# Performance work log

Measured on AMD Instinct MI355X. Metric: run time of the kernel, lower is better.

The kernel has to match this reference:

```python
import jax, jax.numpy as jnp
import numpy as np

B, S, HID = 1, 2048, 2048
H = 16
DN, DR, DV = 128, 64, 128          # qk_nope_head_dim, qk_rope_head_dim, v_head_dim
DQ = DN + DR                        # q_head_dim = 192
QLR, KVLR = 1536, 512               # q_lora_rank, kv_lora_rank
MAXP = 32 * 1024
SCALE = DQ ** -0.5
EPS = 1e-6


def rmsnorm(x, w):
    return x * jax.lax.rsqrt(jnp.mean(x * x, axis=-1, keepdims=True) + EPS) * w


def rotate_half(x):
    h = x.shape[-1] // 2
    return jnp.concatenate((-x[..., h:], x[..., :h]), axis=-1)


def interleave_to_half(x):
    # torch: view(b,h,s,d//2,2).transpose(4,3).reshape(b,h,s,d)
    b, h, s, d = x.shape
    return x.reshape(b, h, s, d // 2, 2).transpose(0, 1, 2, 4, 3).reshape(b, h, s, d)


def setup_inputs() -> dict:
    key = jax.random.key(0)
    ks = jax.random.split(key, 8)
    def w(k, shape):
        fan_in = shape[-1]
        return jax.random.normal(k, shape, jnp.float32) * (fan_in ** -0.5)
    inp = {
        "hidden_states": jax.random.normal(ks[0], (B, S, HID), jnp.float32),
        "q_a_w": w(ks[1], (QLR, HID)),
        "q_a_ln": jnp.ones((QLR,), jnp.float32),
        "q_b_w": w(ks[2], (H * DQ, QLR)),
        "kv_a_w": w(ks[3], (KVLR + DR, HID)),
        "kv_a_ln": jnp.ones((KVLR,), jnp.float32),
        "kv_b_w": w(ks[4], (H * (DN + DV), KVLR)),
        "o_w": w(ks[5], (HID, H * DV)),
    }
    # rotary tables, seq_len = 32k
    inv_freq = 1.0 / (10000.0 ** (np.arange(0, DR, 2, dtype=np.float32) / DR))
    t = np.arange(MAXP, dtype=np.float32)
    freqs = np.outer(t, inv_freq)
    emb = np.concatenate((freqs, freqs), axis=-1)
    inp["cos"] = jnp.asarray(np.cos(emb), jnp.float32)
    inp["sin"] = jnp.asarray(np.sin(emb), jnp.float32)
    # bool mask, True = masked (causal)
    inp["attention_mask"] = jnp.triu(jnp.ones((S, S), bool), 1)[None, None]
    inp["position_ids"] = jnp.arange(S, dtype=jnp.int64 if jax.config.jax_enable_x64 else jnp.int32)[None].repeat(B, 0)
    return inp


def reference(hidden_states, q_a_w, q_a_ln, q_b_w, kv_a_w, kv_a_ln, kv_b_w, o_w,
              cos, sin, attention_mask, position_ids):
    b, s, _ = hidden_states.shape
    # low-rank Q: q_b(LN(q_a(x)))
    q = rmsnorm(hidden_states @ q_a_w.T, q_a_ln) @ q_b_w.T         # [b,s,H*DQ]
    q = q.reshape(b, s, H, DQ).transpose(0, 2, 1, 3)               # [b,H,s,DQ]
    q_nope, q_pe = q[..., :DN], q[..., DN:]
    # compressed KV + decoupled rope key
    ckv = hidden_states @ kv_a_w.T                                  # [b,s,KVLR+DR]
    compressed_kv, k_pe = ckv[..., :KVLR], ckv[..., KVLR:]
    k_pe = k_pe.reshape(b, s, 1, DR).transpose(0, 2, 1, 3)          # [b,1,s,DR]
    kv = rmsnorm(compressed_kv, kv_a_ln) @ kv_b_w.T                 # [b,s,H*(DN+DV)]
    kv = kv.reshape(b, s, H, DN + DV).transpose(0, 2, 1, 3)         # [b,H,s,DN+DV]
    k_nope, value_states = kv[..., :DN], kv[..., DN:]
    # rotary with interleaved->half reorder on the rope slice only
    cos_p = cos[position_ids][:, None]                              # [b,1,s,DR]
    sin_p = sin[position_ids][:, None]
    q_pe = interleave_to_half(q_pe)
    k_pe = interleave_to_half(k_pe)
    q_pe = q_pe * cos_p + rotate_half(q_pe) * sin_p
    k_pe = k_pe * cos_p + rotate_half(k_pe) * sin_p
    query_states = jnp.concatenate((q_nope, q_pe), axis=-1)         # [b,H,s,DQ]
    key_states = jnp.concatenate(
        (k_nope, jnp.broadcast_to(k_pe, (b, H, s, DR))), axis=-1)   # [b,H,s,DQ]
    # manual attention
    scores = jnp.einsum("bhqd,bhkd->bhqk", query_states, key_states) * SCALE
    scores = jnp.where(attention_mask, jnp.float32(-10000.0), scores)
    attn = jax.nn.softmax(scores.astype(jnp.float32), axis=-1).astype(query_states.dtype)
    attn_out = jnp.einsum("bhqk,bhkd->bhqd", attn, value_states)    # [b,H,s,DV]
    attn_out = attn_out.transpose(0, 2, 1, 3).reshape(b, s, H * DV)
    return attn_out @ o_w.T                                         # [b,s,HID]
```

## Files before the change

kernel.cpp:

```cpp
#include <hip/hip_runtime.h>
#include <stdint.h>

typedef unsigned short u16;
typedef __attribute__((ext_vector_type(8))) short short8;
typedef __attribute__((ext_vector_type(4))) float f32x4;
typedef __attribute__((ext_vector_type(4))) unsigned short ushort4_t;
typedef __attribute__((ext_vector_type(4))) float float4_t;

#define DEV_INLINE __device__ __forceinline__

DEV_INLINE u16 f2bf(float f) {
    union { float f; unsigned u; } x; x.f = f;
    unsigned u = x.u;
    unsigned r = (u + 0x7FFFu + ((u >> 16) & 1u)) >> 16;
    return (u16)r;
}

DEV_INLINE float bf2f(u16 b) {
    union { unsigned u; float f; } x; x.u = ((unsigned)b) << 16;
    return x.f;
}

DEV_INLINE float fexp2(float x) {
    float r;
    asm("v_exp_f32 %0, %1" : "=v"(r) : "v"(x));
    return r;
}

DEV_INLINE unsigned cvtpk_bf16(float lo, float hi) {
    unsigned r;
    asm("v_cvt_pk_bf16_f32 %0, %1, %2" : "=v"(r) : "v"(lo), "v"(hi));
    return r;
}

template <int CTRL>
DEV_INLINE float dppmax(float x) {
    union { float f; int i; } u; u.f = x;
    int y = __builtin_amdgcn_update_dpp(u.i, u.i, CTRL, 0xf, 0xf, true);
    union { int i; float f; } v; v.i = y;
    return fmaxf(x, v.f);
}

DEV_INLINE float rmax16(float x) {
    x = dppmax<0xB1>(x);
    x = dppmax<0x4E>(x);
    x = dppmax<0x141>(x);
    x = dppmax<0x140>(x);
    return x;
}

__global__ void conv_multi(const float* __restrict__ s0, u16* __restrict__ d0, long e0,
                           const float* __restrict__ s1, u16* __restrict__ d1, long e1,
                           const float* __restrict__ s2, u16* __restrict__ d2, long e2,
                           const float* __restrict__ s3, u16* __restrict__ d3, long e3,
                           const float* __restrict__ s4, u16* __restrict__ d4, long e4) {
    long i = (long)blockIdx.x * 256 + threadIdx.x;
    const float* s; u16* d; long base;
    if      (i < e0) { s = s0; d = d0; base = 0; }
    else if (i < e1) { s = s1; d = d1; base = e0; }
    else if (i < e2) { s = s2; d = d2; base = e1; }
    else if (i < e3) { s = s3; d = d3; base = e2; }
    else if (i < e4) { s = s4; d = d4; base = e3; }
    else return;
    long j = i - base;
    float4_t v = ((const float4_t*)s)[j];
    ushort4_t o;
    o.x = f2bf(v.x); o.y = f2bf(v.y); o.z = f2bf(v.z); o.w = f2bf(v.w);
    ((ushort4_t*)d)[j] = o;
}

__global__ void conv_pad(const float* __restrict__ in, u16* __restrict__ out,
                         int rows_valid, long n4, int cols4) {
    long i = (long)blockIdx.x * blockDim.x + threadIdx.x;
    if (i >= n4) return;
    long row = i / cols4;
    ushort4_t o; o.x = 0; o.y = 0; o.z = 0; o.w = 0;
    if (row < rows_valid) {
        float4_t v = ((const float4_t*)in)[i];
        o.x = f2bf(v.x); o.y = f2bf(v.y); o.z = f2bf(v.z); o.w = f2bf(v.w);
    }
    ((ushort4_t*)out)[i] = o;
}

#define BK 32

DEV_INLINE void gload16(const u16* g, u16* l) {
    __builtin_amdgcn_global_load_lds((const __attribute__((address_space(1))) unsigned int*)g,
                                     (__attribute__((address_space(3))) unsigned int*)l,
                                     16, 0, 0);
}

template <typename OT>
__global__ __launch_bounds__(256) void gemm64_db(const u16* __restrict__ A, const u16* __restrict__ B,
                                                 OT* __restrict__ C, int M, int N, int K) {
    __shared__ u16 As[2][64 * BK];
    __shared__ u16 Bs[2][128 * BK];
    const int tid = threadIdx.x;
    const int wid = tid >> 6, lane = tid & 63;
    const int lm = lane & 15, lk = lane >> 4;
    const long bm = (long)blockIdx.y * 64, bn = (long)blockIdx.x * 128;

    f32x4 acc[4][2] = {};

    const int rowS = lane >> 2;
    const int colS = ((lane & 3) ^ ((lane >> 3) & 3)) * 8;
    const int cs = (lm >> 1) & 3;
    const u16* Ag = A + (bm + wid * 16 + rowS) * (long)K + colS;
    const u16* Bg = B + (bn + wid * 32 + rowS) * (long)K + colS;
    const int aoff = wid * 16 * BK;
    const int boff = wid * 32 * BK;

    gload16(Ag, &As[0][aoff]);
    gload16(Bg, &Bs[0][boff]);
    gload16(Bg + 16 * (long)K, &Bs[0][boff + 16 * BK]);
    __syncthreads();

    int cur = 0;
    for (int k0 = 0; k0 < K; k0 += BK) {
        if (k0 + BK < K) {
            gload16(Ag + k0 + BK, &As[cur ^ 1][aoff]);
            gload16(Bg + k0 + BK, &Bs[cur ^ 1][boff]);
            gload16(Bg + 16 * (long)K + k0 + BK, &Bs[cur ^ 1][boff + 16 * BK]);
        }
        short8 af[4], bfr[2];
#pragma unroll
        for (int m = 0; m < 4; ++m)
            af[m] = *(const short8*)&As[cur][(m * 16 + lm) * BK + (lk ^ cs) * 8];
#pragma unroll
        for (int n = 0; n < 2; ++n)
            bfr[n] = *(const short8*)&Bs[cur][(wid * 32 + n * 16 + lm) * BK + (lk ^ cs) * 8];
#pragma unroll
        for (int m = 0; m < 4; ++m)
#pragma unroll
            for (int n = 0; n < 2; ++n)
                acc[m][n] = __builtin_amdgcn_mfma_f32_16x16x32_bf16(af[m], bfr[n], acc[m][n], 0, 0, 0);
        __syncthreads();
        cur ^= 1;
    }

#pragma unroll
    for (int m = 0; m < 4; ++m)
#pragma unroll
        for (int n = 0; n < 2; ++n)
#pragma unroll
            for (int r = 0; r < 4; ++r) {
                long idx = (bm + m * 16 + lk * 4 + r) * (long)N + bn + wid * 32 + n * 16 + lm;
                if constexpr (sizeof(OT) == 4) C[idx] = acc[m][n][r];
                else                           C[idx] = f2bf(acc[m][n][r]);
            }
}

__global__ __launch_bounds__(256) void rmsnorm_bf16(const float* __restrict__ in, const float* __restrict__ w,
                                                    u16* __restrict__ out, int ldin, int ldout, int ncols) {
    const int row = blockIdx.x, tid = threadIdx.x;
    const float* x = in + (long)row * ldin;
    float ss = 0.f;
    for (int c = tid; c < ncols; c += 256) { float v = x[c]; ss = fmaf(v, v, ss); }
#pragma unroll
    for (int off = 32; off > 0; off >>= 1) ss += __shfl_down(ss, off);
    __shared__ float part[4];
    if ((tid & 63) == 0) part[tid >> 6] = ss;
    __syncthreads();
    float tot = part[0] + part[1] + part[2] + part[3];
    float rs = rsqrtf(tot / (float)ncols + 1e-6f);
    for (int c = tid; c < ncols; c += 256) out[(long)row * ldout + c] = f2bf(x[c] * rs * w[c]);
}

__global__ void rope_k(const float* __restrict__ ckv, const int* __restrict__ pos,
                       const float* __restrict__ cosT, const float* __restrict__ sinT,
                       u16* __restrict__ Kb) {
    int idx = blockIdx.x * 256 + threadIdx.x;
    if (idx >= 2048 * 32) return;
    int s = idx >> 5, j = idx & 31;
    long p = pos[s];
    const float* row = ckv + (long)s * 2176 + 2048;
    float x0 = row[2 * j], x1 = row[2 * j + 1];
    float c0 = cosT[p * 64 + j],      s0 = sinT[p * 64 + j];
    float c1 = cosT[p * 64 + 32 + j], s1 = sinT[p * 64 + 32 + j];
    u16 o0 = f2bf(x0 * c0 - x1 * s0);
    u16 o1 = f2bf(x1 * c1 + x0 * s1);
#pragma unroll
    for (int h = 0; h < 16; ++h) {
        u16* kr = Kb + ((long)h * 2048 + s) * 192 + 128;
        kr[j] = o0; kr[32 + j] = o1;
    }
}

__global__ void build_q(const u16* __restrict__ q, const int* __restrict__ pos,
                        const float* __restrict__ cosT, const float* __restrict__ sinT,
                        u16* __restrict__ Qb) {
    long idx = (long)blockIdx.x * 256 + threadIdx.x;
    if (idx >= 16L * 2048 * 192) return;
    int d = (int)(idx % 192);
    int s = (int)((idx / 192) % 2048);
    int h = (int)(idx / (192L * 2048));
    const u16* qrow = q + (long)s * 3072 + h * 192;
    u16 outv;
    if (d < 128) {
        outv = qrow[d];
    } else {
        long p = pos[s];
        int dd = d - 128;
        float cv = cosT[p * 64 + dd], sv = sinT[p * 64 + dd];
        float val;
        if (dd < 32) val = bf2f(qrow[128 + 2 * dd]) * cv - bf2f(qrow[128 + 2 * dd + 1]) * sv;
        else { int jj = dd - 32; val = bf2f(qrow[128 + 2 * jj + 1]) * cv + bf2f(qrow[128 + 2 * jj]) * sv; }
        outv = f2bf(val);
    }
    Qb[((long)h * 2048 + s) * 192 + d] = outv;
}

__global__ __launch_bounds__(256) void build_kv2(const u16* __restrict__ kv, u16* __restrict__ Kb,
                                                 u16* __restrict__ Vt) {
    __shared__ u16 Ls[128][72];
    const int h = blockIdx.y, s0 = blockIdx.x * 64;
    const int tid = threadIdx.x;
#pragma unroll
    for (int i = 0; i < 8; ++i) {
        int u = i * 256 + tid;
        int r = u >> 5, c8 = (u & 31) * 8;
        short8 x = *(const short8*)(kv + (long)(s0 + r) * 4096 + h * 256 + c8);
        if (c8 < 128) {
            *(short8*)(Kb + ((long)h * 2048 + s0 + r) * 192 + c8) = x;
        } else {
#pragma unroll
            for (int j = 0; j < 8; ++j) {
                int d = c8 - 128 + j;
                Ls[d][r ^ (((d >> 3) & 7) << 3)] = (u16)x[j];
            }
        }
    }
    __syncthreads();
#pragma unroll
    for (int i = 0; i < 8; ++i) {
        int u = i * 256 + tid;
        int d = u >> 4, s4 = (u & 15) * 4;
        int swz = ((d >> 3) & 7) << 3;
        ushort4_t v;
        v.x = Ls[d][(s4 + 0) ^ swz]; v.y = Ls[d][(s4 + 1) ^ swz];
        v.z = Ls[d][(s4 + 2) ^ swz]; v.w = Ls[d][(s4 + 3) ^ swz];
        *(ushort4_t*)(Vt + ((long)h * 128 + d) * 2048 + s0 + s4) = v;
    }
}

__global__ __launch_bounds__(512) void attn_fwd(const u16* __restrict__ Qb, const u16* __restrict__ Kb,
                                                const u16* __restrict__ Vt, u16* __restrict__ Ao) {
    __shared__ __align__(16) char smem[94720];

    const int b = blockIdx.x;
    const int h = (b & 7) * 2 + ((b >> 3) & 1);
    const int pi = b >> 4;
    const int tid = threadIdx.x;
    const int wid = tid >> 6, lane = tid & 63;
    const int lm = lane & 15, lk = lane >> 4;
    const int s = wid >> 2, wp = wid & 3;
    const int t256 = tid & 255;

    u16* Ks0 = (u16*)smem + s * 12800;
    u16* Vs0 = (u16*)(smem + 51200) + s * 8192;
    u16* PsW = (u16*)(smem + 83968) + wid * 640;
    float* ML = (float*)(smem + 94208);
    float* Ob = (float*)smem;

    const u16* Kh = Kb + (long)h * 2048 * 192;
    const u16* Vh = Vt + (long)h * 128 * 2048;

    short8 bones = {};
    if (lm == 0) {
#pragma unroll
        for (int j = 0; j < 8; ++j) bones[j] = (short)0x3F80;
    }
    const float C2 = 0.104117548f;

    for (int half = 0; half < 2; ++half) {
        const int qi = half ? (31 - pi) : pi;
        const int q0 = qi * 64;
        const int nt = 2 * qi + 2;
        const int niter = qi + 1;

        short8 qf[6];
        const u16* qbase = Qb + ((long)h * 2048 + q0 + wp * 16 + lm) * 192;
#pragma unroll
        for (int kf = 0; kf < 6; ++kf) qf[kf] = *(const short8*)(qbase + kf * 32 + lk * 8);

        f32x4 o[8] = {};
        f32x4 o9 = {};
        float mrow[4] = {-1e30f, -1e30f, -1e30f, -1e30f};

        short8 kreg[3], vreg[2];
        {
            const long k0 = s * 32;
#pragma unroll
            for (int i = 0; i < 3; ++i) {
                int idx = i * 256 + t256; int r = idx / 24, c = (idx % 24) * 8;
                kreg[i] = *(const short8*)(Kh + (k0 + r) * 192 + c);
            }
#pragma unroll
            for (int i = 0; i < 2; ++i) {
                int idx = i * 256 + t256; int dv = idx >> 2, kvb = idx & 3;
                vreg[i] = *(const short8*)(Vh + (long)dv * 2048 + k0 + kvb * 8);
            }
#pragma unroll
            for (int i = 0; i < 3; ++i) {
                int idx = i * 256 + t256; int r = idx / 24, c = (idx % 24) * 8;
                *(short8*)&Ks0[r * 200 + c] = kreg[i];
            }
#pragma unroll
            for (int i = 0; i < 2; ++i) {
                int idx = i * 256 + t256; int dv = idx >> 2, kvb = idx & 3;
                *(short8*)&Vs0[kvb * 1024 + ((dv * 8) ^ (kvb * 16))] = vreg[i];
            }
        }
        __syncthreads();

        int cur = 0;
        for (int it = 0; it < niter; ++it) {
            const int ts = 2 * it + s;
            const int k0 = ts * 32;
            const bool more = (it + 1 < niter);

            if (more) {
                const long k0n = (long)(ts + 2) * 32;
#pragma unroll
                for (int i = 0; i < 3; ++i) {
                    int idx = i * 256 + t256; int r = idx / 24, c = (idx % 24) * 8;
                    kreg[i] = *(const short8*)(Kh + (k0n + r) * 192 + c);
                }
#pragma unroll
                for (int i = 0; i < 2; ++i) {
                    int idx = i * 256 + t256; int dv = idx >> 2, kvb = idx & 3;
                    vreg[i] = *(const short8*)(Vh + (long)dv * 2048 + k0n + kvb * 8);
                }
            }

            const u16* KsC = Ks0 + cur * 6400;
            const u16* VsC = Vs0 + cur * 4096;

            f32x4 sfr[2] = {};
#pragma unroll
            for (int n = 0; n < 2; ++n)
#pragma unroll
                for (int kf = 0; kf < 6; ++kf) {
                    short8 kb = *(const short8*)&KsC[(n * 16 + lm) * 200 + kf * 32 + lk * 8];
                    sfr[n] = __builtin_amdgcn_mfma_f32_16x16x32_bf16(qf[kf], kb, sfr[n], 0, 0, 0);
                }

            float sv[2][4];
            const bool bt = (ts >= nt - 2);
#pragma unroll
            for (int n = 0; n < 2; ++n)
#pragma unroll
                for (int r = 0; r < 4; ++r) {
                    float val = sfr[n][r] * C2;
                    if (bt && (k0 + n * 16 + lm > q0 + wp * 16 + lk * 4 + r)) val = -1e30f;
                    sv[n][r] = val;
                }

            float pmax[4];
#pragma unroll
            for (int r = 0; r < 4; ++r)
                pmax[r] = rmax16(fmaxf(sv[0][r], sv[1][r]));
            bool need = (pmax[0] > mrow[0] + 8.f) || (pmax[1] > mrow[1] + 8.f) ||
                        (pmax[2] > mrow[2] + 8.f) || (pmax[3] > mrow[3] + 8.f);
            if (__any(need)) {
#pragma unroll
                for (int r = 0; r < 4; ++r) {
                    float mnew = fmaxf(mrow[r], pmax[r]);
                    float alpha = fexp2(mrow[r] - mnew);
                    mrow[r] = mnew;
#pragma unroll
                    for (int d = 0; d < 8; ++d) o[d][r] *= alpha;
                    o9[r] *= alpha;
                }
            }
#pragma unroll
            for (int n = 0; n < 2; ++n) {
                float p0 = fexp2(sv[n][0] - mrow[0]);
                float p1 = fexp2(sv[n][1] - mrow[1]);
                float p2 = fexp2(sv[n][2] - mrow[2]);
                float p3 = fexp2(sv[n][3] - mrow[3]);
                unsigned pk01 = cvtpk_bf16(p0, p1);
                unsigned pk23 = cvtpk_bf16(p2, p3);
                int rb = (lk * 4) * 40 + n * 16 + lm;
                PsW[rb]       = (u16)pk01;
                PsW[rb + 40]  = (u16)(pk01 >> 16);
                PsW[rb + 80]  = (u16)pk23;
                PsW[rb + 120] = (u16)(pk23 >> 16);
            }

            short8 pf = *(const short8*)&PsW[lm * 40 + lk * 8];
#pragma unroll
            for (int d = 0; d < 8; ++d) {
                short8 vf = *(const short8*)&VsC[lk * 1024 + (((d * 16 + lm) * 8) ^ (lk * 16))];
                o[d] = __builtin_amdgcn_mfma_f32_16x16x32_bf16(pf, vf, o[d], 0, 0, 0);
            }
            o9 = __builtin_amdgcn_mfma_f32_16x16x32_bf16(pf, bones, o9, 0, 0, 0);

            if (more) {
                u16* KsN = Ks0 + (cur ^ 1) * 6400;
                u16* VsN = Vs0 + (cur ^ 1) * 4096;
#pragma unroll
                for (int i = 0; i < 3; ++i) {
                    int idx = i * 256 + t256; int r = idx / 24, c = (idx % 24) * 8;
                    *(short8*)&KsN[r * 200 + c] = kreg[i];
                }
#pragma unroll
                for (int i = 0; i < 2; ++i) {
                    int idx = i * 256 + t256; int dv = idx >> 2, kvb = idx & 3;
                    *(short8*)&VsN[kvb * 1024 + ((dv * 8) ^ (kvb * 16))] = vreg[i];
                }
            }
            __syncthreads();
            cur ^= 1;
        }

        if (s == 1) {
#pragma unroll
            for (int d = 0; d < 8; ++d)
#pragma unroll
                for (int r = 0; r < 4; ++r)
                    Ob[(wp * 16 + lk * 4 + r) * 128 + d * 16 + lm] = o[d][r];
            if (lm == 0) {
#pragma unroll
                for (int r = 0; r < 4; ++r) {
                    int row = wp * 16 + lk * 4 + r;
                    ML[row * 2 + 0] = mrow[r];
                    ML[row * 2 + 1] = o9[r];
                }
            }
        }
        __syncthreads();
        if (s == 0) {
            float e0[4], e1[4], invl[4];
#pragma unroll
            for (int r = 0; r < 4; ++r) {
                int row = wp * 16 + lk * 4 + r;
                float m1 = ML[row * 2 + 0];
                float l1 = ML[row * 2 + 1];
                float l0 = __shfl(o9[r], lane & 48);
                float M = fmaxf(mrow[r], m1);
                e0[r] = fexp2(mrow[r] - M);
                e1[r] = fexp2(m1 - M);
                invl[r] = 1.f / (l0 * e0[r] + l1 * e1[r]);
            }
#pragma unroll
            for (int d = 0; d < 8; ++d)
#pragma unroll
                for (int r = 0; r < 4; ++r) {
                    int row = wp * 16 + lk * 4 + r;
                    float val = (o[d][r] * e0[r] +
                                 Ob[row * 128 + d * 16 + lm] * e1[r]) * invl[r];
                    Ao[((long)q0 + row) * 2048 + h * 128 + d * 16 + lm] = f2bf(val);
                }
        }
        __syncthreads();
    }
}

extern "C" void kernel_launch(void* const* d_in, const int* in_sizes, int n_in,
                              void* d_out, int out_size, void* d_ws, size_t ws_size,
                              hipStream_t stream) {
    (void)in_sizes; (void)n_in; (void)out_size; (void)ws_size;
    const float* hidden  = (const float*)d_in[0];
    const float* q_a_w   = (const float*)d_in[1];
    const float* q_a_ln  = (const float*)d_in[2];
    const float* q_b_w   = (const float*)d_in[3];
    const float* kv_a_w  = (const float*)d_in[4];
    const float* kv_a_ln = (const float*)d_in[5];
    const float* kv_b_w  = (const float*)d_in[6];
    const float* o_w     = (const float*)d_in[7];
    const float* cosT    = (const float*)d_in[8];
    const float* sinT    = (const float*)d_in[9];
    const int*   pos     = (const int*)d_in[11];

    char* ws = (char*)d_ws;
    u16* o_w_bf   = (u16*)(ws + 0);
    u16* qb_w_bf  = (u16*)(ws + 8388608);
    u16* kvb_w_bf = (u16*)(ws + 17825792);
    u16* qn_bf    = (u16*)(ws + 22020096);
    u16* kvn_bf   = (u16*)(ws + 28311552);
    u16* Qb       = (u16*)(ws + 30408704);
    u16* Kb       = (u16*)(ws + 42991616);
    u16* Vt       = (u16*)(ws + 55574528);
    u16* aout_bf  = (u16*)(ws + 63963136);
    u16*   hid_bf    = (u16*)(ws + 72351744);
    u16*   qkva_w_bf = (u16*)(ws + 80740352);
    float* qkva_f    = (float*)(ws + 89653248);
    u16*   q_f_bf    = (u16*)(ws + 72351744);
    u16*   kv_f_bf   = (u16*)(ws + 89653248);

    conv_multi<<<17920, 256, 0, stream>>>(
        hidden, hid_bf,    1048576L,
        q_a_w,  qkva_w_bf, 1835008L,
        q_b_w,  qb_w_bf,   3014656L,
        kv_b_w, kvb_w_bf,  3538944L,
        o_w,    o_w_bf,    4587520L);
    conv_pad<<<(640L*2048/4 + 255)/256, 256, 0, stream>>>(kv_a_w, qkva_w_bf + 1536L*2048, 576, 640L*2048/4, 512);

    gemm64_db<float><<<dim3(17, 32), 256, 0, stream>>>(hid_bf, qkva_w_bf, qkva_f, 2048, 2176, 2048);

    rmsnorm_bf16<<<2048, 256, 0, stream>>>(qkva_f, q_a_ln, qn_bf, 2176, 1536, 1536);
    rmsnorm_bf16<<<2048, 256, 0, stream>>>(qkva_f + 1536, kv_a_ln, kvn_bf, 2176, 512, 512);
    rope_k<<<(2048*32)/256, 256, 0, stream>>>(qkva_f, pos, cosT, sinT, Kb);

    gemm64_db<u16><<<dim3(24, 32), 256, 0, stream>>>(qn_bf, qb_w_bf, q_f_bf, 2048, 3072, 1536);
    gemm64_db<u16><<<dim3(32, 32), 256, 0, stream>>>(kvn_bf, kvb_w_bf, kv_f_bf, 2048, 4096, 512);

    build_q<<<(unsigned)((16L*2048*192 + 255)/256), 256, 0, stream>>>(q_f_bf, pos, cosT, sinT, Qb);
    build_kv2<<<dim3(32, 16), 256, 0, stream>>>(kv_f_bf, Kb, Vt);

    attn_fwd<<<256, 512, 0, stream>>>(Qb, Kb, Vt, aout_bf);

    gemm64_db<float><<<dim3(16, 32), 256, 0, stream>>>(aout_bf, o_w_bf, (float*)d_out, 2048, 2048, 2048);
}
```

Before: 246.2 us.

## Use 128x128 GEMM tiles, split-K output projection, and swizzled K smem in attention

Adds a 128x128-tile double-buffered GEMM with an optional split-K template parameter. The q_b and kv_b projections now use it, and the output projection uses split-K=2 into two fp32 partial buffers summed by a new add kernel. The attention kernel's K shared-memory layout drops its padded stride in favour of an XOR swizzle, which cuts LDS usage while aiming to avoid bank conflicts. Larger tiles raise data reuse but halve the block count. Split-K restores parallelism at the cost of extra fp32 traffic and one more launch.

```diff
diff --git a/kernel.cpp b/kernel.cpp
--- a/kernel.cpp
+++ b/kernel.cpp
@@ -82,6 +82,16 @@
     ((ushort4_t*)out)[i] = o;
 }
 
+__global__ void add2_f32(const float* __restrict__ a, const float* __restrict__ b,
+                         float* __restrict__ c, long n4) {
+    long i = (long)blockIdx.x * 256 + threadIdx.x;
+    if (i >= n4) return;
+    float4_t x = ((const float4_t*)a)[i];
+    float4_t y = ((const float4_t*)b)[i];
+    x.x += y.x; x.y += y.y; x.z += y.z; x.w += y.w;
+    ((float4_t*)c)[i] = x;
+}
+
 #define BK 32
 
 DEV_INLINE void gload16(const u16* g, u16* l) {
@@ -147,6 +157,72 @@
                 long idx = (bm + m * 16 + lk * 4 + r) * (long)N + bn + wid * 32 + n * 16 + lm;
                 if constexpr (sizeof(OT) == 4) C[idx] = acc[m][n][r];
                 else                           C[idx] = f2bf(acc[m][n][r]);
+            }
+}
+
+template <typename OT, int SPLITK>
+__global__ __launch_bounds__(256) void gemm128_db(const u16* __restrict__ A, const u16* __restrict__ B,
+                                                  OT* __restrict__ C, int M, int N, int K) {
+    __shared__ u16 As[2][128 * BK];
+    __shared__ u16 Bs[2][128 * BK];
+    const int tid = threadIdx.x;
+    const int wid = tid >> 6, lane = tid & 63;
+    const int lm = lane & 15, lk = lane >> 4;
+    const int wr = wid >> 1, wc = wid & 1;
+    const long bm = (long)blockIdx.y * 128, bn = (long)blockIdx.x * 128;
+    const int Kh = K / SPLITK;
+    const long kbase = (long)blockIdx.z * Kh;
+    OT* Cp = C + (long)blockIdx.z * M * (long)N;
+
+    f32x4 acc[4][4] = {};
+
+    const int rowS = lane >> 2;
+    const int colS = ((lane & 3) ^ ((lane >> 3) & 3)) * 8;
+    const int cs = (lm >> 1) & 3;
+    const u16* Ag = A + (bm + wid * 16 + rowS) * (long)K + kbase + colS;
+    const u16* Bg = B + (bn + wid * 16 + rowS) * (long)K + kbase + colS;
+    const int off0 = wid * 512;
+    const int off1 = off0 + 64 * 32;
+
+    gload16(Ag, &As[0][off0]);
+    gload16(Ag + 64 * (long)K, &As[0][off1]);
+    gload16(Bg, &Bs[0][off0]);
+    gload16(Bg + 64 * (long)K, &Bs[0][off1]);
+    __syncthreads();
+
+    int cur = 0;
+    for (int k0 = 0; k0 < Kh; k0 += BK) {
+        if (k0 + BK < Kh) {
+            gload16(Ag + k0 + BK, &As[cur ^ 1][off0]);
+            gload16(Ag + 64 * (long)K + k0 + BK, &As[cur ^ 1][off1]);
+            gload16(Bg + k0 + BK, &Bs[cur ^ 1][off0]);
+            gload16(Bg + 64 * (long)K + k0 + BK, &Bs[cur ^ 1][off1]);
+        }
+        short8 af[4], bfr[4];
+#pragma unroll
+        for (int m = 0; m < 4; ++m)
+            af[m] = *(const short8*)&As[cur][(wr * 64 + m * 16 + lm) * BK + (lk ^ cs) * 8];
+#pragma unroll
+        for (int n = 0; n < 4; ++n)
+            bfr[n] = *(const short8*)&Bs[cur][(wc * 64 + n * 16 + lm) * BK + (lk ^ cs) * 8];
+#pragma unroll
+        for (int m = 0; m < 4; ++m)
+#pragma unroll
+            for (int n = 0; n < 4; ++n)
+                acc[m][n] = __builtin_amdgcn_mfma_f32_16x16x32_bf16(af[m], bfr[n], acc[m][n], 0, 0, 0);
+        __syncthreads();
+        cur ^= 1;
+    }
+
+#pragma unroll
+    for (int m = 0; m < 4; ++m)
+#pragma unroll
+        for (int n = 0; n < 4; ++n)
+#pragma unroll
+            for (int r = 0; r < 4; ++r) {
+                long idx = (bm + wr * 64 + m * 16 + lk * 4 + r) * (long)N + bn + wc * 64 + n * 16 + lm;
+                if constexpr (sizeof(OT) == 4) Cp[idx] = acc[m][n][r];
+                else                           Cp[idx] = f2bf(acc[m][n][r]);
             }
 }
 
@@ -245,7 +321,7 @@
 
 __global__ __launch_bounds__(512) void attn_fwd(const u16* __restrict__ Qb, const u16* __restrict__ Kb,
                                                 const u16* __restrict__ Vt, u16* __restrict__ Ao) {
-    __shared__ __align__(16) char smem[94720];
+    __shared__ __align__(16) char smem[92672];
 
     const int b = blockIdx.x;
     const int h = (b & 7) * 2 + ((b >> 3) & 1);
@@ -256,10 +332,10 @@
     const int s = wid >> 2, wp = wid & 3;
     const int t256 = tid & 255;
 
-    u16* Ks0 = (u16*)smem + s * 12800;
-    u16* Vs0 = (u16*)(smem + 51200) + s * 8192;
-    u16* PsW = (u16*)(smem + 83968) + wid * 640;
-    float* ML = (float*)(smem + 94208);
+    u16* Ks0 = (u16*)smem + s * 12288;
+    u16* Vs0 = (u16*)(smem + 49152) + s * 8192;
+    u16* PsW = (u16*)(smem + 81920) + wid * 640;
+    float* ML = (float*)(smem + 92160);
     float* Ob = (float*)smem;
 
     const u16* Kh = Kb + (long)h * 2048 * 192;
@@ -302,8 +378,8 @@
             }
 #pragma unroll
             for (int i = 0; i < 3; ++i) {
-                int idx = i * 256 + t256; int r = idx / 24, c = (idx % 24) * 8;
-                *(short8*)&Ks0[r * 200 + c] = kreg[i];
+                int idx = i * 256 + t256; int r = idx / 24, c8 = idx % 24;
+                *(short8*)&Ks0[r * 192 + ((c8 ^ (r & 7)) << 3)] = kreg[i];
             }
 #pragma unroll
             for (int i = 0; i < 2; ++i) {
@@ -333,7 +409,7 @@
                 }
             }
 
-            const u16* KsC = Ks0 + cur * 6400;
+            const u16* KsC = Ks0 + cur * 6144;
             const u16* VsC = Vs0 + cur * 4096;
 
             f32x4 sfr[2] = {};
@@ -341,7 +417,7 @@
             for (int n = 0; n < 2; ++n)
 #pragma unroll
                 for (int kf = 0; kf < 6; ++kf) {
-                    short8 kb = *(const short8*)&KsC[(n * 16 + lm) * 200 + kf * 32 + lk * 8];
+                    short8 kb = *(const short8*)&KsC[(n * 16 + lm) * 192 + (((kf * 4 + lk) ^ (lm & 7)) << 3)];
                     sfr[n] = __builtin_amdgcn_mfma_f32_16x16x32_bf16(qf[kf], kb, sfr[n], 0, 0, 0);
                 }
 
@@ -397,12 +473,12 @@
             o9 = __builtin_amdgcn_mfma_f32_16x16x32_bf16(pf, bones, o9, 0, 0, 0);
 
             if (more) {
-                u16* KsN = Ks0 + (cur ^ 1) * 6400;
+                u16* KsN = Ks0 + (cur ^ 1) * 6144;
                 u16* VsN = Vs0 + (cur ^ 1) * 4096;
 #pragma unroll
                 for (int i = 0; i < 3; ++i) {
-                    int idx = i * 256 + t256; int r = idx / 24, c = (idx % 24) * 8;
-                    *(short8*)&KsN[r * 200 + c] = kreg[i];
+                    int idx = i * 256 + t256; int r = idx / 24, c8 = idx % 24;
+                    *(short8*)&KsN[r * 192 + ((c8 ^ (r & 7)) << 3)] = kreg[i];
                 }
 #pragma unroll
                 for (int i = 0; i < 2; ++i) {
@@ -488,6 +564,8 @@
     float* qkva_f    = (float*)(ws + 89653248);
     u16*   q_f_bf    = (u16*)(ws + 72351744);
     u16*   kv_f_bf   = (u16*)(ws + 89653248);
+    float* op0       = (float*)(ws + 107479040);
+    float* op1       = (float*)(ws + 124256256);
 
     conv_multi<<<17920, 256, 0, stream>>>(
         hidden, hid_bf,    1048576L,
@@ -503,13 +581,14 @@
     rmsnorm_bf16<<<2048, 256, 0, stream>>>(qkva_f + 1536, kv_a_ln, kvn_bf, 2176, 512, 512);
     rope_k<<<(2048*32)/256, 256, 0, stream>>>(qkva_f, pos, cosT, sinT, Kb);
 
-    gemm64_db<u16><<<dim3(24, 32), 256, 0, stream>>>(qn_bf, qb_w_bf, q_f_bf, 2048, 3072, 1536);
-    gemm64_db<u16><<<dim3(32, 32), 256, 0, stream>>>(kvn_bf, kvb_w_bf, kv_f_bf, 2048, 4096, 512);
+    gemm128_db<u16, 1><<<dim3(24, 16), 256, 0, stream>>>(qn_bf, qb_w_bf, q_f_bf, 2048, 3072, 1536);
+    gemm128_db<u16, 1><<<dim3(32, 16), 256, 0, stream>>>(kvn_bf, kvb_w_bf, kv_f_bf, 2048, 4096, 512);
 
     build_q<<<(unsigned)((16L*2048*192 + 255)/256), 256, 0, stream>>>(q_f_bf, pos, cosT, sinT, Qb);
     build_kv2<<<dim3(32, 16), 256, 0, stream>>>(kv_f_bf, Kb, Vt);
 
     attn_fwd<<<256, 512, 0, stream>>>(Qb, Kb, Vt, aout_bf);
 
-    gemm64_db<float><<<dim3(16, 32), 256, 0, stream>>>(aout_bf, o_w_bf, (float*)d_out, 2048, 2048, 2048);
-}
+    gemm128_db<float, 2><<<dim3(16, 16, 2), 256, 0, stream>>>(aout_bf, o_w_bf, op0, 2048, 2048, 2048);
+    add2_f32<<<4096, 256, 0, stream>>>(op0, op1, (float*)d_out, 2048L*2048/4);
+}
```

Result: no change. 248.7 us (+1.0%).
